# Optimization experiments

Hardware: AMD Instinct MI355X
Metric: run time of the kernel (lower is better)

Reference implementation:

```python
import jax, jax.numpy as jnp
import numpy as np

THETA = 0.7
KS = 3          # deformable-conv kernel size
N = KS * KS     # 9 sampling points


def setup_inputs() -> dict:
    key = jax.random.key(0)
    k = jax.random.split(key, 7)
    B, C, H, W = 2, 256, 64, 64
    x = jax.random.normal(k[0], (B, C, H, W), jnp.float32)
    # offset-predicting conv (3x3, pad 1), 2*N output channels; small init so offsets are sane
    p_w = jax.random.normal(k[1], (2 * N, C, 3, 3), jnp.float32) * 0.01
    p_b = jax.random.normal(k[2], (2 * N,), jnp.float32) * 0.01
    # modulation conv (3x3, pad 1), N output channels
    m_w = jax.random.normal(k[3], (N, C, 3, 3), jnp.float32) * 0.01
    m_b = jnp.zeros((N,), jnp.float32)
    # final deform conv weight (applied as ks x ks, stride ks over the unfolded map), no bias
    dconv_w = jax.random.normal(k[4], (256, C, KS, KS), jnp.float32) * 0.05
    # central-difference conv raw weight, shape (Cout, Cin, 1, 5), no bias
    cdc_w = jax.random.normal(k[5], (256, C, 1, 5), jnp.float32) * 0.05
    return {"x": x, "p_w": p_w, "p_b": p_b, "m_w": m_w, "m_b": m_b,
            "dconv_w": dconv_w, "cdc_w": cdc_w}


def _conv2d(x, w, pad):
    return jax.lax.conv_general_dilated(
        x, w, window_strides=(1, 1), padding=pad,
        dimension_numbers=("NCHW", "OIHW", "NCHW"))


def deform_conv(x, p_w, p_b, m_w, m_b, dconv_w):
    B, C, H, W = x.shape
    same = [(1, 1), (1, 1)]
    offset = _conv2d(x, p_w, same) + p_b[None, :, None, None]          # [B,2N,H,W]
    m = jax.nn.sigmoid(_conv2d(x, m_w, same) + m_b[None, :, None, None])  # [B,N,H,W]

    xp = jnp.pad(x, ((0, 0), (0, 0), (1, 1), (1, 1)))  # zero padding 1
    Hp, Wp = H + 2, W + 2

    # p = p_0 + p_n + offset  (x = row coord, y = col coord; torch meshgrid 'ij')
    p_n_x = jnp.repeat(jnp.arange(-1, 2, dtype=x.dtype), 3)   # [-1,-1,-1,0,0,0,1,1,1]
    p_n_y = jnp.tile(jnp.arange(-1, 2, dtype=x.dtype), 3)     # [-1,0,1,-1,0,1,-1,0,1]
    rows = jnp.arange(1, H + 1, dtype=x.dtype)                # p_0_x
    cols = jnp.arange(1, W + 1, dtype=x.dtype)                # p_0_y
    px = offset[:, :N] + p_n_x[None, :, None, None] + rows[None, None, :, None]
    py = offset[:, N:] + p_n_y[None, :, None, None] + cols[None, None, None, :]
    px = jnp.transpose(px, (0, 2, 3, 1))  # [B,H,W,N]
    py = jnp.transpose(py, (0, 2, 3, 1))

    # integer corners from UNCLAMPED p (detached), as in the original
    fx = jnp.floor(jax.lax.stop_gradient(px))
    fy = jnp.floor(jax.lax.stop_gradient(py))
    qx0 = jnp.clip(fx, 0, Hp - 1)
    qy0 = jnp.clip(fy, 0, Wp - 1)
    qx1 = jnp.clip(fx + 1, 0, Hp - 1)
    qy1 = jnp.clip(fy + 1, 0, Wp - 1)

    # clamp p before computing bilinear weights (original order)
    pxc = jnp.clip(px, 0, Hp - 1)
    pyc = jnp.clip(py, 0, Wp - 1)
    g_lt = (1 + (qx0 - pxc)) * (1 + (qy0 - pyc))
    g_rb = (1 - (qx1 - pxc)) * (1 - (qy1 - pyc))
    g_lb = (1 + (qx0 - pxc)) * (1 - (qy1 - pyc))
    g_rt = (1 - (qx1 - pxc)) * (1 + (qy0 - pyc))

    xf = xp.reshape(B, C, Hp * Wp)

    def gather(qx, qy):
        idx = (qx.astype(jnp.int32) * Wp + qy.astype(jnp.int32)).reshape(B, 1, -1)
        return jnp.take_along_axis(xf, idx, axis=2).reshape(B, C, H, W, N)

    x_off = (g_lt[:, None] * gather(qx0, qy0)
             + g_rb[:, None] * gather(qx1, qy1)
             + g_lb[:, None] * gather(qx0, qy1)
             + g_rt[:, None] * gather(qx1, qy0))          # [B,C,H,W,N]
    x_off = x_off * jnp.transpose(m, (0, 2, 3, 1))[:, None]  # modulation broadcast over C

    # conv(ksxks, stride ks) over the unfolded map == contraction over the N taps;
    # tap n = 3r + c corresponds to kernel position (r, c)
    w = dconv_w.reshape(dconv_w.shape[0], C, N)
    return jnp.einsum("bchwn,ocn->bohw", x_off, w)


def cdc_conv(x, cdc_w):
    Co, Ci = cdc_w.shape[0], cdc_w.shape[1]
    z = jnp.zeros((Co, Ci, 1), cdc_w.dtype)
    wk = jnp.concatenate(
        [z, cdc_w[:, :, :, 0], z, cdc_w[:, :, :, 1], cdc_w[:, :, :, 2],
         cdc_w[:, :, :, 3], z, cdc_w[:, :, :, 4], z], axis=2
    ).reshape(Co, Ci, 3, 3)
    out_normal = _conv2d(x, wk, [(1, 1), (1, 1)])
    kdiff = cdc_w.sum(axis=(2, 3))[:, :, None, None]
    out_diff = _conv2d(x, kdiff, [(0, 0), (0, 0)])
    return out_normal - THETA * out_diff


def reference(x, p_w, p_b, m_w, m_b, dconv_w, cdc_w):
    out_dc = jax.nn.relu(deform_conv(x, p_w, p_b, m_w, m_b, dconv_w))
    out_cdc = jax.nn.relu(cdc_conv(x, cdc_w))
    return jnp.concatenate([out_dc, out_cdc], axis=1)  # [B,512,H,W]
```

## Files before the change

### kernel.cpp

```cpp
#include <hip/hip_runtime.h>
#include <hip/hip_bf16.h>
#include <math.h>

#define XT_BSTRIDE (66*66*256)
#define THETA_ 0.7f

typedef unsigned short u16;
typedef __attribute__((ext_vector_type(8))) short bf16x8;
typedef __attribute__((ext_vector_type(4))) float f32x4;

#define GLOAD16(gp, lp) __builtin_amdgcn_global_load_lds( \
    (const __attribute__((address_space(1))) unsigned int*)(gp), \
    (__attribute__((address_space(3))) unsigned int*)(lp), 16, 0, 0)

#define WAIT_VMCNT(N) asm volatile("s_waitcnt vmcnt(" #N ")" ::: "memory")

__device__ __forceinline__ void bar_fenced() {
  __builtin_amdgcn_sched_barrier(0);
  __builtin_amdgcn_s_barrier();
  __builtin_amdgcn_sched_barrier(0);
}

__device__ __forceinline__ float bf2f(u16 v) {
  union { unsigned u; float f; } x; x.u = ((unsigned)v) << 16; return x.f;
}
__device__ __forceinline__ u16 f2bf(float f) {
  __hip_bfloat16 h = __float2bfloat16(f);
  return *(u16*)&h;
}

__device__ __forceinline__ size_t swz_idx(int row, int k, int KT) {
  int kt = k >> 6, kc = (k >> 3) & 7, kj = k & 7;
  return (size_t)row * KT + kt * 64 + ((kc ^ (row & 7)) << 3) + kj;
}

__global__ __launch_bounds__(256) void prep(
    const float* __restrict__ x, const float* __restrict__ p_w,
    const float* __restrict__ m_w, const float* __restrict__ dconv_w,
    const float* __restrict__ cdc_w, u16* __restrict__ xTb,
    u16* __restrict__ W1t, u16* __restrict__ Wdt, u16* __restrict__ Wct) {
  int blk = blockIdx.x;
  if (blk < 512) {
    int cg = blk & 3;
    int h  = (blk >> 2) & 63;
    int b  = blk >> 8;
    __shared__ float tile[64][65];
    const float* xp = x + ((size_t)(b * 256 + cg * 64)) * 4096 + h * 64;
#pragma unroll
    for (int j = 0; j < 16; j++) {
      int idx = j * 256 + threadIdx.x;
      int ci = idx >> 6, w = idx & 63;
      tile[ci][w] = xp[(size_t)ci * 4096 + w];
    }
    __syncthreads();
    u16* xo = xTb + (size_t)b * XT_BSTRIDE + ((h + 1) * 66 + 1) * 256 + cg * 64;
#pragma unroll
    for (int j = 0; j < 16; j++) {
      int idx = j * 256 + threadIdx.x;
      int w = idx >> 6, ci = idx & 63;
      xo[(size_t)w * 256 + ci] = f2bf(tile[ci][w]);
    }
    return;
  }
  if (blk < 1032) {
    int i = (blk - 512) * 256 + threadIdx.x;
    if (i >= 133120) return;
    int c = i & 255;
    int j = i >> 8;
    int b = (j >= 260) ? 1 : 0;
    int r = j - b * 260;
    int hp, wp;
    if (r < 66)       { hp = 0;        wp = r; }
    else if (r < 132) { hp = 65;       wp = r - 66; }
    else if (r < 196) { hp = r - 131;  wp = 0; }
    else              { hp = r - 195;  wp = 65; }
    xTb[(size_t)b * XT_BSTRIDE + (hp * 66 + wp) * 256 + c] = 0;
    return;
  }
  int i = (blk - 1032) * 256 + threadIdx.x;
  if (i < 73728) {
    int o = i / 2304, k = i % 2304;
    int kp = k >> 8, c = k & 255;
    float v = 0.f;
    if (o < 18)      v = p_w[((size_t)o * 256 + c) * 9 + kp];
    else if (o < 27) v = m_w[((size_t)(o - 18) * 256 + c) * 9 + kp];
    W1t[swz_idx(o, k, 2304)] = f2bf(v);
    return;
  }
  int j = i - 73728;
  if (j < 589824) {
    int o = j / 2304, k = j % 2304;
    int n = k >> 8, c = k & 255;
    Wdt[swz_idx(o, k, 2304)] = f2bf(dconv_w[((size_t)o * 256 + c) * 9 + n]);
    return;
  }
  int j2 = j - 589824;
  if (j2 < 327680) {
    int o = j2 / 1280, k = j2 % 1280;
    int t = k >> 8, c = k & 255;
    const float* cw = cdc_w + ((size_t)o * 256 + c) * 5;
    float v = cw[t];
    if (t == 2) v -= THETA_ * (cw[0] + cw[1] + cw[2] + cw[3] + cw[4]);
    Wct[swz_idx(o, k, 1280)] = f2bf(v);
  }
}

__global__ __launch_bounds__(256) void sample_params(
    const float* __restrict__ omp, const float* __restrict__ p_b,
    const float* __restrict__ m_b, int4* __restrict__ sidx,
    float4* __restrict__ sg) {
  int i = blockIdx.x * 256 + threadIdx.x;
  if (i >= 73728) return;
  int n = i % 9;
  int p = i / 9;
  int b = p >> 12;
  int hw = p & 4095;
  int h = hw >> 6, w = hw & 63;
  float offx = p_b[n], offy = p_b[9 + n], mraw = m_b[n];
#pragma unroll
  for (int ks = 0; ks < 4; ks++) {
    const float* base = omp + ks * 221184 + b * 110592;
    offx += base[(size_t)n * 4096 + hw];
    offy += base[(size_t)(9 + n) * 4096 + hw];
    mraw += base[(size_t)(18 + n) * 4096 + hw];
  }
  float px = offx + (float)(h + n / 3);
  float py = offy + (float)(w + n % 3);
  float fx = floorf(px), fy = floorf(py);
  float qx0 = fminf(fmaxf(fx, 0.f), 65.f);
  float qy0 = fminf(fmaxf(fy, 0.f), 65.f);
  float qx1 = fminf(fmaxf(fx + 1.f, 0.f), 65.f);
  float qy1 = fminf(fmaxf(fy + 1.f, 0.f), 65.f);
  float pxc = fminf(fmaxf(px, 0.f), 65.f);
  float pyc = fminf(fmaxf(py, 0.f), 65.f);
  float gx0 = 1.f + (qx0 - pxc);
  float gx1 = 1.f - (qx1 - pxc);
  float gy0 = 1.f + (qy0 - pyc);
  float gy1 = 1.f - (qy1 - pyc);
  float m = 1.f / (1.f + expf(-mraw));
  sidx[i] = make_int4((int)qx0 * 66 + (int)qy0, (int)qx1 * 66 + (int)qy1,
                      (int)qx0 * 66 + (int)qy1, (int)qx1 * 66 + (int)qy0);
  sg[i] = make_float4(gx0 * gy0 * m, gx1 * gy1 * m, gx0 * gy1 * m, gx1 * gy0 * m);
}

__global__ __launch_bounds__(256) void gather_Ad(const u16* __restrict__ xTb,
                                                 const int4* __restrict__ sidx,
                                                 const float4* __restrict__ sg,
                                                 u16* __restrict__ Ad) {
  int gid = blockIdx.x * 256 + threadIdx.x;
  int q = gid & 31;
  int s = gid >> 5;
  int p = s / 9, n = s - p * 9;
  int b = p >> 12;
  int4 qi = sidx[s];
  float4 g = sg[s];
  const u16* xb = xTb + (size_t)b * XT_BSTRIDE + q * 8;
  bf16x8 a0 = *(const bf16x8*)(xb + (size_t)qi.x * 256);
  bf16x8 a1 = *(const bf16x8*)(xb + (size_t)qi.y * 256);
  bf16x8 a2 = *(const bf16x8*)(xb + (size_t)qi.z * 256);
  bf16x8 a3 = *(const bf16x8*)(xb + (size_t)qi.w * 256);
  bf16x8 ov;
#pragma unroll
  for (int j = 0; j < 8; j++) {
    float v = g.x * bf2f((u16)a0[j]) + g.y * bf2f((u16)a1[j]) +
              g.z * bf2f((u16)a2[j]) + g.w * bf2f((u16)a3[j]);
    ov[j] = (short)f2bf(v);
  }
  int k = n * 256 + q * 8;
  int kt = k >> 6, kc = (k >> 3) & 7;
  *(bf16x8*)(Ad + (size_t)p * 2304 + kt * 64 + (((kc ^ (p & 7)) << 3))) = ov;
}

template <int KTOT, int MODE>
__device__ __forceinline__ void gemm_body(
    const u16* __restrict__ Asrc, const u16* __restrict__ Bt,
    float* __restrict__ outp, int mt, int nt, u16* As, u16* Bs) {
  const int NKT = KTOT / 64;
  const int OCH0 = (MODE == 1) ? 256 : 0;
  int tid = threadIdx.x;
  int wid = tid >> 6, lane = tid & 63;
  int wr = wid >> 1, wc = wid & 1;
  int pbase = mt * 128;
  int obase = nt * 64;
  int l8 = lane >> 3, l7 = lane & 7;
  int lr = lane & 15, lg = lane >> 4;

  f32x4 acc[2][4];
#pragma unroll
  for (int i = 0; i < 2; i++)
#pragma unroll
    for (int j = 0; j < 4; j++) acc[i][j] = {0.f, 0.f, 0.f, 0.f};

  const int dh1[5] = {0, 1, 1, 1, 2}, dw1[5] = {1, 0, 1, 2, 1};

  auto stage = [&](int kt, u16* Ah, u16* Bh) {
    if (MODE == 0) {
#pragma unroll
      for (int i = 0; i < 4; i++) {
        int r0 = wid * 32 + i * 8;
        const u16* g = Asrc + (size_t)(pbase + r0 + l8) * KTOT + kt * 64 + (l7 << 3);
        GLOAD16(g, &Ah[r0 * 64]);
      }
    } else {
      int t = kt >> 2, c0 = (kt & 3) << 6;
      int dh = dh1[t], dw = dw1[t];
#pragma unroll
      for (int i = 0; i < 4; i++) {
        int r0 = wid * 32 + i * 8;
        int r = r0 + l8;
        int p = pbase + r;
        int b = p >> 12, hw = p & 4095, h = hw >> 6, w = hw & 63;
        int chunk = l7 ^ (r & 7);
        const u16* g = Asrc + (size_t)b * XT_BSTRIDE +
                       ((h + dh) * 66 + (w + dw)) * 256 + c0 + (chunk << 3);
        GLOAD16(g, &Ah[r0 * 64]);
      }
    }
#pragma unroll
    for (int i = 0; i < 2; i++) {
      int o0 = wid * 16 + i * 8;
      const u16* g = Bt + (size_t)(obase + o0 + l8) * KTOT + kt * 64 + (l7 << 3);
      GLOAD16(g, &Bh[o0 * 64]);
    }
  };

  stage(0, As, Bs);

  for (int it = 0; it < NKT; it++) {
    int cur = it & 1;
    u16* Ac = As + cur * 8192;
    u16* Bc = Bs + cur * 4096;

    bar_fenced();
    if (it + 1 < NKT) {
      stage(it + 1, As + (cur ^ 1) * 8192, Bs + (cur ^ 1) * 4096);
      WAIT_VMCNT(6);
    } else {
      WAIT_VMCNT(0);
    }
    bar_fenced();

    bf16x8 av[4][2], bv[2][2];
#pragma unroll
    for (int mf = 0; mf < 4; mf++) {
      int r = wr * 64 + mf * 16 + lr;
#pragma unroll
      for (int ks = 0; ks < 2; ks++) {
        int kc = ks * 4 + lg;
        av[mf][ks] = *(const bf16x8*)&Ac[r * 64 + ((kc ^ (r & 7)) << 3)];
      }
    }
#pragma unroll
    for (int nf = 0; nf < 2; nf++) {
      int o = wc * 32 + nf * 16 + lr;
#pragma unroll
      for (int ks = 0; ks < 2; ks++) {
        int kc = ks * 4 + lg;
        bv[nf][ks] = *(const bf16x8*)&Bs[cur * 4096 + o * 64 + ((kc ^ (o & 7)) << 3)];
      }
    }
#pragma unroll
    for (int nf = 0; nf < 2; nf++)
#pragma unroll
      for (int mf = 0; mf < 4; mf++)
#pragma unroll
        for (int ks = 0; ks < 2; ks++)
          acc[nf][mf] = __builtin_amdgcn_mfma_f32_16x16x32_bf16(
              bv[nf][ks], av[mf][ks], acc[nf][mf], 0, 0, 0);
  }

#pragma unroll
  for (int nf = 0; nf < 2; nf++)
#pragma unroll
    for (int mf = 0; mf < 4; mf++) {
      int p = pbase + wr * 64 + mf * 16 + lr;
      int hw = p & 4095, b = p >> 12;
      int og = OCH0 + obase + wc * 32 + nf * 16 + lg * 4;
      f32x4 v = acc[nf][mf];
#pragma unroll
      for (int e = 0; e < 4; e++)
        outp[(size_t)(b * 512 + og + e) * 4096 + hw] = fmaxf(v[e], 0.f);
    }
}

__device__ __forceinline__ void offmod_body(
    const u16* __restrict__ xTb, const u16* __restrict__ Bt,
    float* __restrict__ outp, int mt, int kt0, int nkt, u16* As, u16* Bs) {
  int tid = threadIdx.x;
  int wid = tid >> 6, lane = tid & 63;
  int pbase = mt * 128;
  int l8 = lane >> 3, l7 = lane & 7;
  int lr = lane & 15, lg = lane >> 4;

  f32x4 acc[2][2];
#pragma unroll
  for (int i = 0; i < 2; i++)
#pragma unroll
    for (int j = 0; j < 2; j++) acc[i][j] = {0.f, 0.f, 0.f, 0.f};

  auto stage = [&](int kt, u16* Ah, u16* Bh) {
    int t = kt >> 2, c0 = (kt & 3) << 6;
    int dh = t / 3, dw = t % 3;
#pragma unroll
    for (int i = 0; i < 4; i++) {
      int r0 = wid * 32 + i * 8;
      int r = r0 + l8;
      int p = pbase + r;
      int b = p >> 12, hw = p & 4095, h = hw >> 6, w = hw & 63;
      int chunk = l7 ^ (r & 7);
      const u16* g = xTb + (size_t)b * XT_BSTRIDE +
                     ((h + dh) * 66 + (w + dw)) * 256 + c0 + (chunk << 3);
      GLOAD16(g, &Ah[r0 * 64]);
    }
    {
      int o0 = wid * 8;
      const u16* g = Bt + (size_t)(o0 + l8) * 2304 + kt * 64 + (l7 << 3);
      GLOAD16(g, &Bh[o0 * 64]);
    }
  };

  stage(kt0, As, Bs);

  for (int it = 0; it < nkt; it++) {
    int cur = it & 1;
    u16* Ac = As + cur * 8192;
    u16* Bc = Bs + cur * 2048;

    bar_fenced();
    if (it + 1 < nkt) {
      stage(kt0 + it + 1, As + (cur ^ 1) * 8192, Bs + (cur ^ 1) * 2048);
      WAIT_VMCNT(5);
    } else {
      WAIT_VMCNT(0);
    }
    bar_fenced();

    bf16x8 av[2][2], bv[2][2];
#pragma unroll
    for (int mf = 0; mf < 2; mf++) {
      int r = wid * 32 + mf * 16 + lr;
#pragma unroll
      for (int ks = 0; ks < 2; ks++) {
        int kc = ks * 4 + lg;
        av[mf][ks] = *(const bf16x8*)&Ac[r * 64 + ((kc ^ (r & 7)) << 3)];
      }
    }
#pragma unroll
    for (int nf = 0; nf < 2; nf++) {
      int o = nf * 16 + lr;
#pragma unroll
      for (int ks = 0; ks < 2; ks++) {
        int kc = ks * 4 + lg;
        bv[nf][ks] = *(const bf16x8*)&Bc[o * 64 + ((kc ^ (o & 7)) << 3)];
      }
    }
#pragma unroll
    for (int nf = 0; nf < 2; nf++)
#pragma unroll
      for (int mf = 0; mf < 2; mf++)
#pragma unroll
        for (int ks = 0; ks < 2; ks++)
          acc[nf][mf] = __builtin_amdgcn_mfma_f32_16x16x32_bf16(
              bv[nf][ks], av[mf][ks], acc[nf][mf], 0, 0, 0);
  }

#pragma unroll
  for (int nf = 0; nf < 2; nf++)
#pragma unroll
    for (int mf = 0; mf < 2; mf++) {
      int p = pbase + wid * 32 + mf * 16 + lr;
      int hw = p & 4095, b = p >> 12;
      int o0 = nf * 16 + lg * 4;
      f32x4 v = acc[nf][mf];
#pragma unroll
      for (int e = 0; e < 4; e++) {
        int o = o0 + e;
        if (o < 27)
          outp[(size_t)(b * 27 + o) * 4096 + hw] = v[e];
      }
    }
}

__global__ __launch_bounds__(256) void gemm_offmod(const u16* __restrict__ xTb,
                                                   const u16* __restrict__ W1t,
                                                   float* __restrict__ omp) {
  __shared__ u16 As[2 * 128 * 64];
  __shared__ u16 Bs[2 * 32 * 64];
  int bid = blockIdx.x;
  int xcd = bid & 7;
  int i = bid >> 3;
  int mt = xcd * 8 + (i & 7);
  int ks = i >> 3;
  offmod_body(xTb, W1t, omp + ks * 221184, mt, ks * 9, 9, As, Bs);
}

__global__ __launch_bounds__(256) void gemm_main(const u16* __restrict__ Ad,
                                                 const u16* __restrict__ xTb,
                                                 const u16* __restrict__ Wdt,
                                                 const u16* __restrict__ Wct,
                                                 float* __restrict__ out) {
  __shared__ u16 As[2 * 128 * 64];
  __shared__ u16 Bs[2 * 64 * 64];
  int bid = blockIdx.x;
  if (bid < 256) {
    int xcd = bid & 7;
    int j = bid >> 3;
    gemm_body<2304, 0>(Ad, Wdt, out, xcd * 8 + (j >> 2), j & 3, As, Bs);
  } else {
    int b2 = bid - 256;
    int xcd = b2 & 7;
    int j = b2 >> 3;
    gemm_body<1280, 1>(xTb, Wct, out, xcd * 8 + (j >> 2), j & 3, As, Bs);
  }
}

extern "C" void kernel_launch(void* const* d_in, const int* in_sizes, int n_in,
                              void* d_out, int out_size, void* d_ws, size_t ws_size,
                              hipStream_t stream) {
  (void)in_sizes; (void)n_in; (void)out_size; (void)ws_size;
  const float* x       = (const float*)d_in[0];
  const float* p_w     = (const float*)d_in[1];
  const float* p_b     = (const float*)d_in[2];
  const float* m_w     = (const float*)d_in[3];
  const float* m_b     = (const float*)d_in[4];
  const float* dconv_w = (const float*)d_in[5];
  const float* cdc_w   = (const float*)d_in[6];
  float* out = (float*)d_out;
  char* ws = (char*)d_ws;

  u16*   xTb  = (u16*)(ws);
  float* omp  = (float*)(ws + 4460544);
  u16*   W1t  = (u16*)(ws + 7999488);
  u16*   Wdt  = (u16*)(ws + 8146944);
  u16*   Wct  = (u16*)(ws + 9326592);
  int4*  sidx = (int4*)(ws + 9981952);
  float4* sg  = (float4*)(ws + 11161600);
  u16*   Ad   = (u16*)(ws + 12341248);

  prep<<<4904, 256, 0, stream>>>(x, p_w, m_w, dconv_w, cdc_w, xTb, W1t, Wdt, Wct);
  gemm_offmod<<<256, 256, 0, stream>>>(xTb, W1t, omp);
  sample_params<<<288, 256, 0, stream>>>(omp, p_b, m_b, sidx, sg);
  gather_Ad<<<9216, 256, 0, stream>>>(xTb, sidx, sg, Ad);
  gemm_main<<<512, 256, 0, stream>>>(Ad, xTb, Wdt, Wct, out);
}
```

Baseline: 69.98 us.

## Fuse sampling-param computation into gather and halve main GEMM M-tile

The separate sample_params kernel is folded into gather_Ad, so each thread recomputes its bilinear indices and weights from the summed offset/modulation partials. This removes one launch and the sidx/sg round trip through memory, at the cost of 32 threads redundantly reading the 4 partial sums. The main GEMM tile shrinks from 128x64 to 64x64, giving 1024 blocks that interleave the deform and CDC families, with launch_bounds raised to 4 blocks per CU for occupancy. This trades per-block reuse of the weight tiles for better load balance and latency hiding.

After: 63.03 us, median of 3. 1.11x faster.

```diff
diff --git a/kernel.cpp b/kernel.cpp
--- a/kernel.cpp
+++ b/kernel.cpp
@@ -105,17 +105,19 @@
   }
 }
 
-__global__ __launch_bounds__(256) void sample_params(
-    const float* __restrict__ omp, const float* __restrict__ p_b,
-    const float* __restrict__ m_b, int4* __restrict__ sidx,
-    float4* __restrict__ sg) {
-  int i = blockIdx.x * 256 + threadIdx.x;
-  if (i >= 73728) return;
-  int n = i % 9;
-  int p = i / 9;
+__global__ __launch_bounds__(256) void gather_Ad(const u16* __restrict__ xTb,
+                                                 const float* __restrict__ omp,
+                                                 const float* __restrict__ p_b,
+                                                 const float* __restrict__ m_b,
+                                                 u16* __restrict__ Ad) {
+  int gid = blockIdx.x * 256 + threadIdx.x;
+  int q = gid & 31;
+  int s = gid >> 5;
+  int p = s / 9, n = s - p * 9;
   int b = p >> 12;
   int hw = p & 4095;
   int h = hw >> 6, w = hw & 63;
+
   float offx = p_b[n], offy = p_b[9 + n], mraw = m_b[n];
 #pragma unroll
   for (int ks = 0; ks < 4; ks++) {
@@ -138,32 +140,23 @@
   float gy0 = 1.f + (qy0 - pyc);
   float gy1 = 1.f - (qy1 - pyc);
   float m = 1.f / (1.f + expf(-mraw));
-  sidx[i] = make_int4((int)qx0 * 66 + (int)qy0, (int)qx1 * 66 + (int)qy1,
-                      (int)qx0 * 66 + (int)qy1, (int)qx1 * 66 + (int)qy0);
-  sg[i] = make_float4(gx0 * gy0 * m, gx1 * gy1 * m, gx0 * gy1 * m, gx1 * gy0 * m);
-}
-
-__global__ __launch_bounds__(256) void gather_Ad(const u16* __restrict__ xTb,
-                                                 const int4* __restrict__ sidx,
-                                                 const float4* __restrict__ sg,
-                                                 u16* __restrict__ Ad) {
-  int gid = blockIdx.x * 256 + threadIdx.x;
-  int q = gid & 31;
-  int s = gid >> 5;
-  int p = s / 9, n = s - p * 9;
-  int b = p >> 12;
-  int4 qi = sidx[s];
-  float4 g = sg[s];
+  int i0 = (int)qx0 * 66 + (int)qy0;
+  int i1 = (int)qx1 * 66 + (int)qy1;
+  int i2 = (int)qx0 * 66 + (int)qy1;
+  int i3 = (int)qx1 * 66 + (int)qy0;
+  float g0 = gx0 * gy0 * m, g1 = gx1 * gy1 * m;
+  float g2 = gx0 * gy1 * m, g3 = gx1 * gy0 * m;
+
   const u16* xb = xTb + (size_t)b * XT_BSTRIDE + q * 8;
-  bf16x8 a0 = *(const bf16x8*)(xb + (size_t)qi.x * 256);
-  bf16x8 a1 = *(const bf16x8*)(xb + (size_t)qi.y * 256);
-  bf16x8 a2 = *(const bf16x8*)(xb + (size_t)qi.z * 256);
-  bf16x8 a3 = *(const bf16x8*)(xb + (size_t)qi.w * 256);
+  bf16x8 a0 = *(const bf16x8*)(xb + (size_t)i0 * 256);
+  bf16x8 a1 = *(const bf16x8*)(xb + (size_t)i1 * 256);
+  bf16x8 a2 = *(const bf16x8*)(xb + (size_t)i2 * 256);
+  bf16x8 a3 = *(const bf16x8*)(xb + (size_t)i3 * 256);
   bf16x8 ov;
 #pragma unroll
   for (int j = 0; j < 8; j++) {
-    float v = g.x * bf2f((u16)a0[j]) + g.y * bf2f((u16)a1[j]) +
-              g.z * bf2f((u16)a2[j]) + g.w * bf2f((u16)a3[j]);
+    float v = g0 * bf2f((u16)a0[j]) + g1 * bf2f((u16)a1[j]) +
+              g2 * bf2f((u16)a2[j]) + g3 * bf2f((u16)a3[j]);
     ov[j] = (short)f2bf(v);
   }
   int k = n * 256 + q * 8;
@@ -180,24 +173,24 @@
   int tid = threadIdx.x;
   int wid = tid >> 6, lane = tid & 63;
   int wr = wid >> 1, wc = wid & 1;
-  int pbase = mt * 128;
+  int pbase = mt * 64;
   int obase = nt * 64;
   int l8 = lane >> 3, l7 = lane & 7;
   int lr = lane & 15, lg = lane >> 4;
 
-  f32x4 acc[2][4];
+  f32x4 acc[2][2];
 #pragma unroll
   for (int i = 0; i < 2; i++)
 #pragma unroll
-    for (int j = 0; j < 4; j++) acc[i][j] = {0.f, 0.f, 0.f, 0.f};
+    for (int j = 0; j < 2; j++) acc[i][j] = {0.f, 0.f, 0.f, 0.f};
 
   const int dh1[5] = {0, 1, 1, 1, 2}, dw1[5] = {1, 0, 1, 2, 1};
 
   auto stage = [&](int kt, u16* Ah, u16* Bh) {
     if (MODE == 0) {
 #pragma unroll
-      for (int i = 0; i < 4; i++) {
-        int r0 = wid * 32 + i * 8;
+      for (int i = 0; i < 2; i++) {
+        int r0 = wid * 16 + i * 8;
         const u16* g = Asrc + (size_t)(pbase + r0 + l8) * KTOT + kt * 64 + (l7 << 3);
         GLOAD16(g, &Ah[r0 * 64]);
       }
@@ -205,8 +198,8 @@
       int t = kt >> 2, c0 = (kt & 3) << 6;
       int dh = dh1[t], dw = dw1[t];
 #pragma unroll
-      for (int i = 0; i < 4; i++) {
-        int r0 = wid * 32 + i * 8;
+      for (int i = 0; i < 2; i++) {
+        int r0 = wid * 16 + i * 8;
         int r = r0 + l8;
         int p = pbase + r;
         int b = p >> 12, hw = p & 4095, h = hw >> 6, w = hw & 63;
@@ -228,22 +221,22 @@
 
   for (int it = 0; it < NKT; it++) {
     int cur = it & 1;
-    u16* Ac = As + cur * 8192;
+    u16* Ac = As + cur * 4096;
     u16* Bc = Bs + cur * 4096;
 
     bar_fenced();
     if (it + 1 < NKT) {
-      stage(it + 1, As + (cur ^ 1) * 8192, Bs + (cur ^ 1) * 4096);
-      WAIT_VMCNT(6);
+      stage(it + 1, As + (cur ^ 1) * 4096, Bs + (cur ^ 1) * 4096);
+      WAIT_VMCNT(4);
     } else {
       WAIT_VMCNT(0);
     }
     bar_fenced();
 
-    bf16x8 av[4][2], bv[2][2];
-#pragma unroll
-    for (int mf = 0; mf < 4; mf++) {
-      int r = wr * 64 + mf * 16 + lr;
+    bf16x8 av[2][2], bv[2][2];
+#pragma unroll
+    for (int mf = 0; mf < 2; mf++) {
+      int r = wr * 32 + mf * 16 + lr;
 #pragma unroll
       for (int ks = 0; ks < 2; ks++) {
         int kc = ks * 4 + lg;
@@ -256,13 +249,13 @@
 #pragma unroll
       for (int ks = 0; ks < 2; ks++) {
         int kc = ks * 4 + lg;
-        bv[nf][ks] = *(const bf16x8*)&Bs[cur * 4096 + o * 64 + ((kc ^ (o & 7)) << 3)];
+        bv[nf][ks] = *(const bf16x8*)&Bc[o * 64 + ((kc ^ (o & 7)) << 3)];
       }
     }
 #pragma unroll
     for (int nf = 0; nf < 2; nf++)
 #pragma unroll
-      for (int mf = 0; mf < 4; mf++)
+      for (int mf = 0; mf < 2; mf++)
 #pragma unroll
         for (int ks = 0; ks < 2; ks++)
           acc[nf][mf] = __builtin_amdgcn_mfma_f32_16x16x32_bf16(
@@ -272,8 +265,8 @@
 #pragma unroll
   for (int nf = 0; nf < 2; nf++)
 #pragma unroll
-    for (int mf = 0; mf < 4; mf++) {
-      int p = pbase + wr * 64 + mf * 16 + lr;
+    for (int mf = 0; mf < 2; mf++) {
+      int p = pbase + wr * 32 + mf * 16 + lr;
       int hw = p & 4095, b = p >> 12;
       int og = OCH0 + obase + wc * 32 + nf * 16 + lg * 4;
       f32x4 v = acc[nf][mf];
@@ -394,24 +387,22 @@
   offmod_body(xTb, W1t, omp + ks * 221184, mt, ks * 9, 9, As, Bs);
 }
 
-__global__ __launch_bounds__(256) void gemm_main(const u16* __restrict__ Ad,
-                                                 const u16* __restrict__ xTb,
-                                                 const u16* __restrict__ Wdt,
-                                                 const u16* __restrict__ Wct,
-                                                 float* __restrict__ out) {
-  __shared__ u16 As[2 * 128 * 64];
+__global__ __launch_bounds__(256, 4) void gemm_main(const u16* __restrict__ Ad,
+                                                    const u16* __restrict__ xTb,
+                                                    const u16* __restrict__ Wdt,
+                                                    const u16* __restrict__ Wct,
+                                                    float* __restrict__ out) {
+  __shared__ u16 As[2 * 64 * 64];
   __shared__ u16 Bs[2 * 64 * 64];
   int bid = blockIdx.x;
-  if (bid < 256) {
-    int xcd = bid & 7;
-    int j = bid >> 3;
-    gemm_body<2304, 0>(Ad, Wdt, out, xcd * 8 + (j >> 2), j & 3, As, Bs);
-  } else {
-    int b2 = bid - 256;
-    int xcd = b2 & 7;
-    int j = b2 >> 3;
-    gemm_body<1280, 1>(xTb, Wct, out, xcd * 8 + (j >> 2), j & 3, As, Bs);
-  }
+  int fam = bid & 1;
+  int idx = bid >> 1;
+  int xcd = idx & 7;
+  int j = idx >> 3;
+  int mt = xcd * 16 + (j & 15);
+  int nt = j >> 4;
+  if (fam == 0) gemm_body<2304, 0>(Ad, Wdt, out, mt, nt, As, Bs);
+  else          gemm_body<1280, 1>(xTb, Wct, out, mt, nt, As, Bs);
 }
 
 extern "C" void kernel_launch(void* const* d_in, const int* in_sizes, int n_in,
@@ -433,13 +424,10 @@
   u16*   W1t  = (u16*)(ws + 7999488);
   u16*   Wdt  = (u16*)(ws + 8146944);
   u16*   Wct  = (u16*)(ws + 9326592);
-  int4*  sidx = (int4*)(ws + 9981952);
-  float4* sg  = (float4*)(ws + 11161600);
-  u16*   Ad   = (u16*)(ws + 12341248);
+  u16*   Ad   = (u16*)(ws + 9981952);
 
   prep<<<4904, 256, 0, stream>>>(x, p_w, m_w, dconv_w, cdc_w, xTb, W1t, Wdt, Wct);
   gemm_offmod<<<256, 256, 0, stream>>>(xTb, W1t, omp);
-  sample_params<<<288, 256, 0, stream>>>(omp, p_b, m_b, sidx, sg);
-  gather_Ad<<<9216, 256, 0, stream>>>(xTb, sidx, sg, Ad);
-  gemm_main<<<512, 256, 0, stream>>>(Ad, xTb, Wdt, Wct, out);
-}
+  gather_Ad<<<9216, 256, 0, stream>>>(xTb, omp, p_b, m_b, Ad);
+  gemm_main<<<1024, 256, 0, stream>>>(Ad, xTb, Wdt, Wct, out);
+}
```
